# Kernel tuning notes

Measured on AMD Instinct MI355X. Metric: run time of the kernel, lower is better.

Reference implementation:

```python
import jax, jax.numpy as jnp
import numpy as np

B, C, H, W = 16, 256, 96, 96
S, N = 128, 64  # num_s = 2*num_mid, num_n = num_mid
EPS = 1e-5


def _bn(x, g, b, m, v):
    # inference-mode BatchNorm2d over channel dim of x:[B,C,H,W]
    scale = g / jnp.sqrt(v + EPS)
    return (x - m[:, None, None]) * scale[:, None, None] + b[:, None, None]


def _proj(x, w, b, g, bb, m, v):
    # 1x1 conv + BN + ReLU (Basconv with is_batchnorm=True, kernel=1)
    y = jnp.einsum('bchw,oc->bohw', x, w) + b[:, None, None]
    return jax.nn.relu(_bn(y, g, bb, m, v))


def _gcn(x, w1, b1, w2):
    # x: [B, S, N]. conv1 acts on node dim (Conv1d over num_node channels),
    # residual add, LeakyReLU(0.2), conv2 acts on state dim (bias=False).
    h = jnp.einsum('bsn,mn->bsm', x, w1) + b1  # node mixing
    h = jax.nn.leaky_relu(h + x, 0.2)
    return jnp.einsum('bsn,ts->btn', h, w2)  # state mixing


def setup_inputs() -> dict:
    key = jax.random.key(0)
    ks = list(jax.random.split(key, 32))
    it = iter(ks)

    def nx(shape, s=0.05):
        return jax.random.normal(next(it), shape, jnp.float32) * s

    inp = {"x": jax.random.normal(next(it), (B, C, H, W), jnp.float32)}
    for name, o in [("s", S), ("p", N), ("r", N)]:
        inp[f"w_{name}"] = nx((o, C))
        inp[f"b_{name}"] = nx((o,))
        inp[f"bn_{name}_g"] = 1.0 + nx((o,))
        inp[f"bn_{name}_b"] = nx((o,))
        inp[f"bn_{name}_m"] = nx((o,))
        inp[f"bn_{name}_v"] = 0.5 + jax.random.uniform(next(it), (o,), jnp.float32)
    inp["g1_w1"] = nx((N, N)); inp["g1_b1"] = nx((N,)); inp["g1_w2"] = nx((S, S))
    inp["g2_w1"] = nx((N, N)); inp["g2_b1"] = nx((N,)); inp["g2_w2"] = nx((S, S))
    inp["fc2_w"] = nx((C, S))
    inp["bn_o_g"] = 1.0 + nx((C,))
    inp["bn_o_b"] = nx((C,))
    inp["bn_o_m"] = nx((C,))
    inp["bn_o_v"] = 0.5 + jax.random.uniform(next(it), (C,), jnp.float32)
    return inp


def reference(x, w_s, b_s, bn_s_g, bn_s_b, bn_s_m, bn_s_v,
              w_p, b_p, bn_p_g, bn_p_b, bn_p_m, bn_p_v,
              w_r, b_r, bn_r_g, bn_r_b, bn_r_m, bn_r_v,
              g1_w1, g1_b1, g1_w2, g2_w1, g2_b1, g2_w2,
              fc2_w, bn_o_g, bn_o_b, bn_o_m, bn_o_v):
    HW = H * W
    xs = _proj(x, w_s, b_s, bn_s_g, bn_s_b, bn_s_m, bn_s_v).reshape(B, S, HW)
    xp = _proj(x, w_p, b_p, bn_p_g, bn_p_b, bn_p_m, bn_p_v).reshape(B, N, HW)
    xr = _proj(x, w_r, b_r, bn_r_g, bn_r_b, bn_r_m, bn_r_v).reshape(B, N, HW)
    # project spatial features into latent graph: [B,S,N], normalized by HW
    g = jnp.einsum('bsl,bnl->bsn', xs, xp) * (1.0 / HW)
    g = _gcn(g, g1_w1, g1_b1, g1_w2)
    g = _gcn(g, g2_w1, g2_b1, g2_w2)
    # reproject latent graph back to spatial: [B,S,HW] -> [B,S,H,W]
    y = jnp.einsum('bsn,bnl->bsl', g, xr).reshape(B, S, H, W)
    y = jnp.einsum('bshw,cs->bchw', y, fc2_w)  # fc_2: 1x1 conv, no bias
    return x + _bn(y, bn_o_g, bn_o_b, bn_o_m, bn_o_v)
```

## Files before the change

### kernel.cpp

```cpp
#include <hip/hip_runtime.h>
#include <cstdint>
#include <cstddef>

#define B_ 16
#define C_ 256
#define HW_ 9216
#define S_ 128
#define N_ 64
#define LT_ 144

typedef __attribute__((ext_vector_type(8))) short bf16x8;
typedef __attribute__((ext_vector_type(4))) float f32x4;
typedef __attribute__((ext_vector_type(8))) unsigned short u16x8;

__device__ __forceinline__ unsigned short f2bf(float f) {
    unsigned int u = __builtin_bit_cast(unsigned int, f);
    u += 0x7fffu + ((u >> 16) & 1u);
    return (unsigned short)(u >> 16);
}
__device__ __forceinline__ float bf2f(unsigned short u) {
    unsigned int x = ((unsigned int)u) << 16;
    return __builtin_bit_cast(float, x);
}

__global__ void k0_prep(
    const float* __restrict__ w_s, const float* __restrict__ w_p, const float* __restrict__ w_r,
    const float* __restrict__ b_s, const float* __restrict__ g_s, const float* __restrict__ bb_s,
    const float* __restrict__ m_s, const float* __restrict__ v_s,
    const float* __restrict__ b_p, const float* __restrict__ g_p, const float* __restrict__ bb_p,
    const float* __restrict__ m_p, const float* __restrict__ v_p,
    const float* __restrict__ b_r, const float* __restrict__ g_r, const float* __restrict__ bb_r,
    const float* __restrict__ m_r, const float* __restrict__ v_r,
    const float* __restrict__ og, const float* __restrict__ ob,
    const float* __restrict__ om, const float* __restrict__ ov,
    unsigned short* __restrict__ Wcf, float* __restrict__ pscale, float* __restrict__ pbeta,
    float* __restrict__ oscale, float* __restrict__ obeta)
{
    const int gid = blockIdx.x * 256 + threadIdx.x;
    const int oc = gid >> 8, c = gid & 255;
    const float* wsrc;
    if (oc < 128)      wsrc = w_s + oc * 256;
    else if (oc < 192) wsrc = w_p + (oc - 128) * 256;
    else               wsrc = w_r + (oc - 192) * 256;
    Wcf[(c >> 3) * 2048 + oc * 8 + (c & 7)] = f2bf(wsrc[c]);
    if (gid < 256) {
        int i; const float *bp, *gp, *bbp, *mp, *vp;
        if (gid < 128)      { i = gid;       bp = b_s; gp = g_s; bbp = bb_s; mp = m_s; vp = v_s; }
        else if (gid < 192) { i = gid - 128; bp = b_p; gp = g_p; bbp = bb_p; mp = m_p; vp = v_p; }
        else                { i = gid - 192; bp = b_r; gp = g_r; bbp = bb_r; mp = m_r; vp = v_r; }
        const float sc = gp[i] / sqrtf(vp[i] + 1e-5f);
        pscale[gid] = sc;
        pbeta[gid]  = (bp[i] - mp[i]) * sc + bbp[i];
        const float so = og[gid] / sqrtf(ov[gid] + 1e-5f);
        oscale[gid] = so;
        obeta[gid]  = ob[gid] - om[gid] * so;
    }
}

__global__ void k0b_wbf(
    const float* __restrict__ g1w1, const float* __restrict__ g1w2,
    const float* __restrict__ g2w1, const float* __restrict__ g2w2,
    const float* __restrict__ fc2w, unsigned short* __restrict__ wbf)
{
    const int gid = blockIdx.x * 256 + threadIdx.x;
    float v;
    if (gid < 4096)       v = g1w1[gid];
    else if (gid < 20480) v = g1w2[gid - 4096];
    else if (gid < 24576) v = g2w1[gid - 20480];
    else if (gid < 40960) v = g2w2[gid - 24576];
    else                  v = fc2w[gid - 40960];
    wbf[gid] = f2bf(v);
}

__global__ __launch_bounds__(256, 3) void k1_proj(
    const float* __restrict__ x, const unsigned short* __restrict__ Wcf,
    const float* __restrict__ pscale, const float* __restrict__ pbeta,
    unsigned short* __restrict__ xrt, unsigned short* __restrict__ gpb)
{
    __shared__ unsigned short SH[18432];
    const int t = threadIdx.x;
    const int lane = t & 63;
    const int w = t >> 6;
    const int lt = blockIdx.x;
    const int b  = blockIdx.y;
    const int l0 = lt * 64;
    const float* xb = x + (size_t)b * C_ * HW_;
    const int lf = lane & 15;
    const int q4 = lane >> 4;
    const int kg0 = q4 * 8;
    const int r4 = q4 * 4;

    const int lq = t & 15;
    const int cs = t >> 4;
    const int c0 = cs * 4;

    f32x4 acc[4][4] = {};
    f32x4 Breg[4];

    #pragma unroll
    for (int j = 0; j < 4; ++j)
        Breg[j] = *(const f32x4*)(xb + (size_t)(c0 + j) * HW_ + l0 + lq * 4);

    for (int kt = 0; kt < 4; ++kt) {
        unsigned short* buf = SH + (kt & 1) * 4608;
        #pragma unroll
        for (int r = 0; r < 4; ++r) {
            const int ll = lq * 4 + r;
            ushort4 wv;
            wv.x = f2bf(Breg[0][r]); wv.y = f2bf(Breg[1][r]);
            wv.z = f2bf(Breg[2][r]); wv.w = f2bf(Breg[3][r]);
            *(ushort4*)&buf[ll * 72 + (c0 ^ ((lq & 7) << 3))] = wv;
        }
        __syncthreads();
        if (kt < 3) {
            const int k0n = (kt + 1) * 64;
            #pragma unroll
            for (int j = 0; j < 4; ++j)
                Breg[j] = *(const f32x4*)(xb + (size_t)(k0n + c0 + j) * HW_ + l0 + lq * 4);
        }
        #pragma unroll
        for (int ks = 0; ks < 2; ++ks) {
            const int kg = ks * 32 + kg0;
            bf16x8 al[4], bo[4];
            #pragma unroll
            for (int mi = 0; mi < 4; ++mi) {
                const int rr = mi * 16 + lf;
                al[mi] = *(const bf16x8*)&buf[rr * 72 + (kg ^ (((rr >> 2) & 7) << 3))];
            }
            const int chunk = kt * 8 + ks * 4 + q4;
            #pragma unroll
            for (int ni = 0; ni < 4; ++ni)
                bo[ni] = *(const bf16x8*)(Wcf + (size_t)chunk * 2048 + (w * 64 + ni * 16 + lf) * 8);
            #pragma unroll
            for (int mi = 0; mi < 4; ++mi)
                #pragma unroll
                for (int ni = 0; ni < 4; ++ni)
                    acc[mi][ni] = __builtin_amdgcn_mfma_f32_16x16x32_bf16(al[mi], bo[ni], acc[mi][ni], 0, 0, 0);
        }
        __syncthreads();
    }

    if (w < 3) {
        #pragma unroll
        for (int ni = 0; ni < 4; ++ni) {
            const int oc = w * 64 + ni * 16 + lf;
            const float sc = pscale[oc];
            const float bt = pbeta[oc];
            #pragma unroll
            for (int mi = 0; mi < 4; ++mi) {
                const int lcol = mi * 16 + r4;
                ushort4 pk;
                #pragma unroll
                for (int r = 0; r < 4; ++r) {
                    float y = acc[mi][ni][r] * sc + bt;
                    y = y > 0.f ? y : 0.f;
                    ((unsigned short*)&pk)[r] = f2bf(y);
                }
                *(ushort4*)&SH[oc * 72 + lcol] = pk;
            }
        }
    } else {
        #pragma unroll
        for (int ni = 0; ni < 4; ++ni) {
            const int oc = 192 + ni * 16 + lf;
            const float sc = pscale[oc];
            const float bt = pbeta[oc];
            const int n = ni * 16 + lf;
            #pragma unroll
            for (int mi = 0; mi < 4; ++mi) {
                const int lbase = mi * 16 + r4;
                #pragma unroll
                for (int r = 0; r < 4; ++r) {
                    float y = acc[mi][ni][r] * sc + bt;
                    y = y > 0.f ? y : 0.f;
                    xrt[((size_t)b * HW_ + l0 + lbase + r) * 64 + n] = f2bf(y);
                }
            }
        }
    }
    __syncthreads();

    {
        f32x4 acc2[4][2] = {};
        #pragma unroll
        for (int ks = 0; ks < 2; ++ks) {
            const int kg = ks * 32 + kg0;
            bf16x8 an[4], bs_[2];
            #pragma unroll
            for (int mi = 0; mi < 4; ++mi)
                an[mi] = *(const bf16x8*)&SH[(128 + mi * 16 + lf) * 72 + kg];
            #pragma unroll
            for (int ni = 0; ni < 2; ++ni)
                bs_[ni] = *(const bf16x8*)&SH[(w * 32 + ni * 16 + lf) * 72 + kg];
            #pragma unroll
            for (int mi = 0; mi < 4; ++mi)
                #pragma unroll
                for (int ni = 0; ni < 2; ++ni)
                    acc2[mi][ni] = __builtin_amdgcn_mfma_f32_16x16x32_bf16(an[mi], bs_[ni], acc2[mi][ni], 0, 0, 0);
        }
        unsigned short* gp = gpb + (size_t)(lt * 16 + b) * (S_ * N_);
        #pragma unroll
        for (int ni = 0; ni < 2; ++ni) {
            const int s = w * 32 + ni * 16 + lf;
            #pragma unroll
            for (int mi = 0; mi < 4; ++mi) {
                ushort4 pk;
                #pragma unroll
                for (int r = 0; r < 4; ++r)
                    ((unsigned short*)&pk)[r] = f2bf(acc2[mi][ni][r]);
                *(ushort4*)&gp[s * 64 + mi * 16 + r4] = pk;
            }
        }
    }
}

__global__ __launch_bounds__(256) void kred(
    const unsigned short* __restrict__ gpb, unsigned short* __restrict__ gred)
{
    const int id = blockIdx.x * 256 + threadIdx.x;
    float s0 = 0.f, s1 = 0.f, s2 = 0.f, s3 = 0.f;
    const unsigned short* p = gpb + (size_t)id * 4;
    #pragma unroll 8
    for (int lt = 0; lt < LT_; ++lt) {
        const ushort4 v = *(const ushort4*)(p + (size_t)lt * 16 * (S_ * N_));
        s0 += bf2f(v.x); s1 += bf2f(v.y); s2 += bf2f(v.z); s3 += bf2f(v.w);
    }
    const float inv = 1.0f / (float)HW_;
    ushort4 h;
    h.x = f2bf(s0 * inv); h.y = f2bf(s1 * inv);
    h.z = f2bf(s2 * inv); h.w = f2bf(s3 * inv);
    *(ushort4*)&gred[(size_t)id * 4] = h;
}

__global__ __launch_bounds__(256) void k_gcn(
    const unsigned short* __restrict__ gred, const unsigned short* __restrict__ wbf,
    const float* __restrict__ b1a, const float* __restrict__ b1b,
    unsigned short* __restrict__ hc)
{
    __shared__ unsigned short G[128 * 72];
    __shared__ unsigned short HT[64 * 136];
    __shared__ unsigned short T2[64 * 136];
    const int b = blockIdx.x;
    const int t = threadIdx.x;
    const int lane = t & 63;
    const int w = t >> 6;
    const int lf = lane & 15;
    const int kg0 = (lane >> 4) * 8;
    const int r4 = (lane >> 4) * 4;

    const unsigned short* w1a = wbf;
    const unsigned short* w2a = wbf + 4096;
    const unsigned short* w1b = wbf + 20480;
    const unsigned short* w2b = wbf + 24576;
    const unsigned short* fc2 = wbf + 40960;

    #pragma unroll
    for (int i = 0; i < 4; ++i) {
        const int chunk = t + i * 256;
        const u16x8 v = *(const u16x8*)(gred + (size_t)b * (S_ * N_) + chunk * 8);
        const int s = chunk >> 3, n = (chunk & 7) * 8;
        *(u16x8*)&G[s * 72 + n] = v;
    }
    __syncthreads();

    for (int pass = 0; pass < 2; ++pass) {
        const unsigned short* w1 = pass ? w1b : w1a;
        const unsigned short* w2 = pass ? w2b : w2a;
        const float* b1 = pass ? b1b : b1a;

        {
            f32x4 acc[2][4] = {};
            #pragma unroll
            for (int ks = 0; ks < 2; ++ks) {
                const int kg = ks * 32 + kg0;
                bf16x8 a[2], bv[4];
                #pragma unroll
                for (int mi = 0; mi < 2; ++mi)
                    a[mi] = *(const bf16x8*)&G[(w * 32 + mi * 16 + lf) * 72 + kg];
                #pragma unroll
                for (int ni = 0; ni < 4; ++ni)
                    bv[ni] = *(const bf16x8*)(w1 + (ni * 16 + lf) * 64 + kg);
                #pragma unroll
                for (int mi = 0; mi < 2; ++mi)
                    #pragma unroll
                    for (int ni = 0; ni < 4; ++ni)
                        acc[mi][ni] = __builtin_amdgcn_mfma_f32_16x16x32_bf16(a[mi], bv[ni], acc[mi][ni], 0, 0, 0);
            }
            #pragma unroll
            for (int mi = 0; mi < 2; ++mi) {
                const int s0 = w * 32 + mi * 16 + r4;
                #pragma unroll
                for (int ni = 0; ni < 4; ++ni) {
                    const int m = ni * 16 + lf;
                    const float bm = b1[m];
                    ushort4 pk;
                    #pragma unroll
                    for (int r = 0; r < 4; ++r) {
                        float v = acc[mi][ni][r] + bm + bf2f(G[(s0 + r) * 72 + m]);
                        v = v > 0.f ? v : 0.2f * v;
                        ((unsigned short*)&pk)[r] = f2bf(v);
                    }
                    *(ushort4*)&HT[m * 136 + s0] = pk;
                }
            }
        }
        __syncthreads();

        {
            f32x4 acc[2][4] = {};
            #pragma unroll
            for (int ks = 0; ks < 4; ++ks) {
                const int kg = ks * 32 + kg0;
                bf16x8 a[2], bv[4];
                #pragma unroll
                for (int mi = 0; mi < 2; ++mi)
                    a[mi] = *(const bf16x8*)(w2 + (w * 32 + mi * 16 + lf) * 128 + kg);
                #pragma unroll
                for (int ni = 0; ni < 4; ++ni)
                    bv[ni] = *(const bf16x8*)&HT[(ni * 16 + lf) * 136 + kg];
                #pragma unroll
                for (int mi = 0; mi < 2; ++mi)
                    #pragma unroll
                    for (int ni = 0; ni < 4; ++ni)
                        acc[mi][ni] = __builtin_amdgcn_mfma_f32_16x16x32_bf16(a[mi], bv[ni], acc[mi][ni], 0, 0, 0);
            }
            if (pass == 0) {
                #pragma unroll
                for (int mi = 0; mi < 2; ++mi) {
                    const int t0 = w * 32 + mi * 16 + r4;
                    #pragma unroll
                    for (int ni = 0; ni < 4; ++ni) {
                        const int m = ni * 16 + lf;
                        #pragma unroll
                        for (int r = 0; r < 4; ++r)
                            G[(t0 + r) * 72 + m] = f2bf(acc[mi][ni][r]);
                    }
                }
            } else {
                #pragma unroll
                for (int mi = 0; mi < 2; ++mi) {
                    const int t0 = w * 32 + mi * 16 + r4;
                    #pragma unroll
                    for (int ni = 0; ni < 4; ++ni) {
                        const int m = ni * 16 + lf;
                        ushort4 pk;
                        #pragma unroll
                        for (int r = 0; r < 4; ++r)
                            ((unsigned short*)&pk)[r] = f2bf(acc[mi][ni][r]);
                        *(ushort4*)&T2[m * 136 + t0] = pk;
                    }
                }
            }
        }
        __syncthreads();
    }

    {
        f32x4 acc[4][4] = {};
        #pragma unroll
        for (int ks = 0; ks < 4; ++ks) {
            const int kg = ks * 32 + kg0;
            bf16x8 a[4], bv[4];
            #pragma unroll
            for (int mi = 0; mi < 4; ++mi)
                a[mi] = *(const bf16x8*)(fc2 + (w * 64 + mi * 16 + lf) * 128 + kg);
            #pragma unroll
            for (int ni = 0; ni < 4; ++ni)
                bv[ni] = *(const bf16x8*)&T2[(ni * 16 + lf) * 136 + kg];
            #pragma unroll
            for (int mi = 0; mi < 4; ++mi)
                #pragma unroll
                for (int ni = 0; ni < 4; ++ni)
                    acc[mi][ni] = __builtin_amdgcn_mfma_f32_16x16x32_bf16(a[mi], bv[ni], acc[mi][ni], 0, 0, 0);
        }
        #pragma unroll
        for (int mi = 0; mi < 4; ++mi) {
            const int c0 = w * 64 + mi * 16 + r4;
            #pragma unroll
            for (int ni = 0; ni < 4; ++ni) {
                const int n = ni * 16 + lf;
                #pragma unroll
                for (int r = 0; r < 4; ++r)
                    hc[((size_t)b * 256 + c0 + r) * 64 + n] = f2bf(acc[mi][ni][r]);
            }
        }
    }
}

__global__ __launch_bounds__(256) void k3_out(
    const float* __restrict__ x, const unsigned short* __restrict__ hc,
    const unsigned short* __restrict__ xrt,
    const float* __restrict__ oscale, const float* __restrict__ obeta,
    float* __restrict__ out)
{
    const int t = threadIdx.x;
    const int lane = t & 63;
    const int w = t >> 6;
    const int wr = w >> 1, wc = w & 1;
    const int l0 = blockIdx.x * 128;
    const int moff = blockIdx.y * 128;
    const int b = blockIdx.z;
    const int lf = lane & 15;
    const int q4 = lane >> 4;
    const int kg0 = q4 * 8;
    const int r4 = q4 * 4;

    const unsigned short* hb = hc + (size_t)b * 256 * 64 + (size_t)(moff + wr * 64) * 64;
    const unsigned short* xrb = xrt + ((size_t)b * HW_ + l0 + wc * 64) * 64;

    f32x4 xpre[8];
    #pragma unroll
    for (int p = 0; p < 8; ++p) {
        const int ni = p >> 2, mi = p & 3;
        const int c = moff + wr * 64 + ni * 16 + lf;
        const int l = l0 + wc * 64 + mi * 16 + r4;
        xpre[p] = *(const f32x4*)(x + ((size_t)b * 256 + c) * HW_ + l);
    }

    f32x4 acc[4][4] = {};
    #pragma unroll
    for (int ks = 0; ks < 2; ++ks) {
        const int kg = ks * 32 + kg0;
        bf16x8 al[4], bc[4];
        #pragma unroll
        for (int mi = 0; mi < 4; ++mi)
            al[mi] = *(const bf16x8*)(xrb + (size_t)(mi * 16 + lf) * 64 + kg);
        #pragma unroll
        for (int ni = 0; ni < 4; ++ni)
            bc[ni] = *(const bf16x8*)(hb + (size_t)(ni * 16 + lf) * 64 + kg);
        #pragma unroll
        for (int mi = 0; mi < 4; ++mi)
            #pragma unroll
            for (int ni = 0; ni < 4; ++ni)
                acc[mi][ni] = __builtin_amdgcn_mfma_f32_16x16x32_bf16(al[mi], bc[ni], acc[mi][ni], 0, 0, 0);
    }
    #pragma unroll
    for (int ni = 0; ni < 4; ++ni) {
        const int c = moff + wr * 64 + ni * 16 + lf;
        const float sc = oscale[c];
        const float bt = obeta[c];
        const size_t rowb = ((size_t)b * 256 + c) * HW_;
        #pragma unroll
        for (int mi = 0; mi < 4; ++mi) {
            const int l = l0 + wc * 64 + mi * 16 + r4;
            const f32x4 xv = (ni < 2) ? xpre[ni * 4 + mi]
                                      : *(const f32x4*)(x + rowb + l);
            f32x4 o;
            #pragma unroll
            for (int r = 0; r < 4; ++r)
                o[r] = xv[r] + acc[mi][ni][r] * sc + bt;
            *(f32x4*)(out + rowb + l) = o;
        }
    }
}

extern "C" void kernel_launch(void* const* d_in, const int* in_sizes, int n_in,
                              void* d_out, int out_size, void* d_ws, size_t ws_size,
                              hipStream_t stream) {
    (void)in_sizes; (void)n_in; (void)out_size;
    const float* x     = (const float*)d_in[0];
    const float* w_s   = (const float*)d_in[1];
    const float* b_s   = (const float*)d_in[2];
    const float* g_s   = (const float*)d_in[3];
    const float* bb_s  = (const float*)d_in[4];
    const float* m_s   = (const float*)d_in[5];
    const float* v_s   = (const float*)d_in[6];
    const float* w_p   = (const float*)d_in[7];
    const float* b_p   = (const float*)d_in[8];
    const float* g_p   = (const float*)d_in[9];
    const float* bb_p  = (const float*)d_in[10];
    const float* m_p   = (const float*)d_in[11];
    const float* v_p   = (const float*)d_in[12];
    const float* w_r   = (const float*)d_in[13];
    const float* b_r   = (const float*)d_in[14];
    const float* g_r   = (const float*)d_in[15];
    const float* bb_r  = (const float*)d_in[16];
    const float* m_r   = (const float*)d_in[17];
    const float* v_r   = (const float*)d_in[18];
    const float* g1w1  = (const float*)d_in[19];
    const float* g1b1  = (const float*)d_in[20];
    const float* g1w2  = (const float*)d_in[21];
    const float* g2w1  = (const float*)d_in[22];
    const float* g2b1  = (const float*)d_in[23];
    const float* g2w2  = (const float*)d_in[24];
    const float* fc2w  = (const float*)d_in[25];
    const float* bn_og = (const float*)d_in[26];
    const float* bn_ob = (const float*)d_in[27];
    const float* bn_om = (const float*)d_in[28];
    const float* bn_ov = (const float*)d_in[29];

    char* ws = (char*)d_ws;
    unsigned short* Wcf = (unsigned short*)(ws + 0);
    float* pscale = (float*)(ws + 131072);
    float* pbeta  = (float*)(ws + 132096);
    float* oscale = (float*)(ws + 133120);
    float* obeta  = (float*)(ws + 134144);
    unsigned short* wbf = (unsigned short*)(ws + 135168);
    const size_t o_fix = 135168 + 147456;
    const size_t sz_xrt = (size_t)B_ * HW_ * 64 * 2;
    const size_t sz_gr  = (size_t)B_ * S_ * N_ * 2;
    const size_t sz_hc  = (size_t)B_ * 256 * 64 * 2;
    const size_t sz_gpb = (size_t)LT_ * B_ * S_ * N_ * 2;
    const size_t need_full = o_fix + sz_xrt + sz_gr + sz_hc + sz_gpb;

    unsigned short* xrt  = (unsigned short*)(ws + o_fix);
    unsigned short* gred = (unsigned short*)(ws + o_fix + sz_xrt);
    unsigned short* hc   = (unsigned short*)(ws + o_fix + sz_xrt + sz_gr);
    unsigned short* gpb;
    if (ws_size >= need_full)
        gpb = (unsigned short*)(ws + o_fix + sz_xrt + sz_gr + sz_hc);
    else
        gpb = (unsigned short*)d_out;

    k0_prep<<<256, 256, 0, stream>>>(
        w_s, w_p, w_r,
        b_s, g_s, bb_s, m_s, v_s,
        b_p, g_p, bb_p, m_p, v_p,
        b_r, g_r, bb_r, m_r, v_r,
        bn_og, bn_ob, bn_om, bn_ov,
        Wcf, pscale, pbeta, oscale, obeta);

    k0b_wbf<<<288, 256, 0, stream>>>(g1w1, g1w2, g2w1, g2w2, fc2w, wbf);

    k1_proj<<<dim3(LT_, B_), 256, 0, stream>>>(x, Wcf, pscale, pbeta, xrt, gpb);

    kred<<<128, 256, 0, stream>>>(gpb, gred);

    k_gcn<<<16, 256, 0, stream>>>(gred, wbf, g1b1, g2b1, hc);

    k3_out<<<dim3(72, 2, 16), 256, 0, stream>>>(x, hc, xrt, oscale, obeta, (float*)d_out);
}
```

Baseline: 156.0 us.

## Stage xrt epilogue through LDS for vectorized stores, merge prep kernels

The xr projection results, which were written with scattered 2-byte global stores, are now staged in shared memory (row stride padded to 76) and written out as 16-byte vector stores per row. The second prep kernel that converts the GCN and fc2 weights is folded into k0_prep as extra blocks, removing one launch. Launch bounds for k1_proj rise to 4 blocks per SM. The added LDS space and the occupancy hint could raise register pressure or cause spills.

```diff
diff --git a/kernel.cpp b/kernel.cpp
--- a/kernel.cpp
+++ b/kernel.cpp
@@ -33,9 +33,26 @@
     const float* __restrict__ m_r, const float* __restrict__ v_r,
     const float* __restrict__ og, const float* __restrict__ ob,
     const float* __restrict__ om, const float* __restrict__ ov,
+    const float* __restrict__ g1w1, const float* __restrict__ g1w2,
+    const float* __restrict__ g2w1, const float* __restrict__ g2w2,
+    const float* __restrict__ fc2w,
     unsigned short* __restrict__ Wcf, float* __restrict__ pscale, float* __restrict__ pbeta,
-    float* __restrict__ oscale, float* __restrict__ obeta)
+    float* __restrict__ oscale, float* __restrict__ obeta,
+    unsigned short* __restrict__ wbf)
 {
+    if (blockIdx.x >= 256) {
+        const int gid = (blockIdx.x - 256) * 256 + threadIdx.x;
+        if (gid < 73728) {
+            float v;
+            if (gid < 4096)       v = g1w1[gid];
+            else if (gid < 20480) v = g1w2[gid - 4096];
+            else if (gid < 24576) v = g2w1[gid - 20480];
+            else if (gid < 40960) v = g2w2[gid - 24576];
+            else                  v = fc2w[gid - 40960];
+            wbf[gid] = f2bf(v);
+        }
+        return;
+    }
     const int gid = blockIdx.x * 256 + threadIdx.x;
     const int oc = gid >> 8, c = gid & 255;
     const float* wsrc;
@@ -57,27 +74,12 @@
     }
 }
 
-__global__ void k0b_wbf(
-    const float* __restrict__ g1w1, const float* __restrict__ g1w2,
-    const float* __restrict__ g2w1, const float* __restrict__ g2w2,
-    const float* __restrict__ fc2w, unsigned short* __restrict__ wbf)
-{
-    const int gid = blockIdx.x * 256 + threadIdx.x;
-    float v;
-    if (gid < 4096)       v = g1w1[gid];
-    else if (gid < 20480) v = g1w2[gid - 4096];
-    else if (gid < 24576) v = g2w1[gid - 20480];
-    else if (gid < 40960) v = g2w2[gid - 24576];
-    else                  v = fc2w[gid - 40960];
-    wbf[gid] = f2bf(v);
-}
-
-__global__ __launch_bounds__(256, 3) void k1_proj(
+__global__ __launch_bounds__(256, 4) void k1_proj(
     const float* __restrict__ x, const unsigned short* __restrict__ Wcf,
     const float* __restrict__ pscale, const float* __restrict__ pbeta,
     unsigned short* __restrict__ xrt, unsigned short* __restrict__ gpb)
 {
-    __shared__ unsigned short SH[18432];
+    __shared__ unsigned short SH[19456];
     const int t = threadIdx.x;
     const int lane = t & 63;
     const int w = t >> 6;
@@ -140,45 +142,38 @@
         __syncthreads();
     }
 
-    if (w < 3) {
-        #pragma unroll
-        for (int ni = 0; ni < 4; ++ni) {
-            const int oc = w * 64 + ni * 16 + lf;
-            const float sc = pscale[oc];
-            const float bt = pbeta[oc];
-            #pragma unroll
-            for (int mi = 0; mi < 4; ++mi) {
-                const int lcol = mi * 16 + r4;
-                ushort4 pk;
-                #pragma unroll
-                for (int r = 0; r < 4; ++r) {
-                    float y = acc[mi][ni][r] * sc + bt;
-                    y = y > 0.f ? y : 0.f;
-                    ((unsigned short*)&pk)[r] = f2bf(y);
-                }
-                *(ushort4*)&SH[oc * 72 + lcol] = pk;
-            }
-        }
-    } else {
-        #pragma unroll
-        for (int ni = 0; ni < 4; ++ni) {
-            const int oc = 192 + ni * 16 + lf;
-            const float sc = pscale[oc];
-            const float bt = pbeta[oc];
-            const int n = ni * 16 + lf;
-            #pragma unroll
-            for (int mi = 0; mi < 4; ++mi) {
-                const int lbase = mi * 16 + r4;
-                #pragma unroll
-                for (int r = 0; r < 4; ++r) {
-                    float y = acc[mi][ni][r] * sc + bt;
-                    y = y > 0.f ? y : 0.f;
-                    xrt[((size_t)b * HW_ + l0 + lbase + r) * 64 + n] = f2bf(y);
-                }
-            }
+    #pragma unroll
+    for (int ni = 0; ni < 4; ++ni) {
+        const int oc = w * 64 + ni * 16 + lf;
+        const float sc = pscale[oc];
+        const float bt = pbeta[oc];
+        #pragma unroll
+        for (int mi = 0; mi < 4; ++mi) {
+            const int lcol = mi * 16 + r4;
+            ushort4 pk;
+            #pragma unroll
+            for (int r = 0; r < 4; ++r) {
+                float y = acc[mi][ni][r] * sc + bt;
+                y = y > 0.f ? y : 0.f;
+                ((unsigned short*)&pk)[r] = f2bf(y);
+            }
+            *(ushort4*)&SH[oc * 76 + lcol] = pk;
         }
     }
     __syncthreads();
+
+    {
+        const int l = t >> 2;
+        const int n0 = (t & 3) * 16;
+        u16x8 v0, v1;
+        #pragma unroll
+        for (int j = 0; j < 8; ++j) v0[j] = SH[(192 + n0 + j) * 76 + l];
+        #pragma unroll
+        for (int j = 0; j < 8; ++j) v1[j] = SH[(192 + n0 + 8 + j) * 76 + l];
+        unsigned short* dst = xrt + ((size_t)b * HW_ + l0 + l) * 64 + n0;
+        *(u16x8*)dst = v0;
+        *(u16x8*)(dst + 8) = v1;
+    }
 
     {
         f32x4 acc2[4][2] = {};
@@ -188,10 +183,10 @@
             bf16x8 an[4], bs_[2];
             #pragma unroll
             for (int mi = 0; mi < 4; ++mi)
-                an[mi] = *(const bf16x8*)&SH[(128 + mi * 16 + lf) * 72 + kg];
+                an[mi] = *(const bf16x8*)&SH[(128 + mi * 16 + lf) * 76 + kg];
             #pragma unroll
             for (int ni = 0; ni < 2; ++ni)
-                bs_[ni] = *(const bf16x8*)&SH[(w * 32 + ni * 16 + lf) * 72 + kg];
+                bs_[ni] = *(const bf16x8*)&SH[(w * 32 + ni * 16 + lf) * 76 + kg];
             #pragma unroll
             for (int mi = 0; mi < 4; ++mi)
                 #pragma unroll
@@ -512,15 +507,14 @@
     else
         gpb = (unsigned short*)d_out;
 
-    k0_prep<<<256, 256, 0, stream>>>(
+    k0_prep<<<544, 256, 0, stream>>>(
         w_s, w_p, w_r,
         b_s, g_s, bb_s, m_s, v_s,
         b_p, g_p, bb_p, m_p, v_p,
         b_r, g_r, bb_r, m_r, v_r,
         bn_og, bn_ob, bn_om, bn_ov,
-        Wcf, pscale, pbeta, oscale, obeta);
-
-    k0b_wbf<<<288, 256, 0, stream>>>(g1w1, g1w2, g2w1, g2w2, fc2w, wbf);
+        g1w1, g1w2, g2w1, g2w2, fc2w,
+        Wcf, pscale, pbeta, oscale, obeta, wbf);
 
     k1_proj<<<dim3(LT_, B_), 256, 0, stream>>>(x, Wcf, pscale, pbeta, xrt, gpb);
 
```

Measured after the change: 153.3 us. Within noise of the previous version (-1.7%).
